# Kernel optimization log

Hardware: AMD Instinct MI355X
Metric: run time of the kernel (lower is better)

## Reference

```python
import jax, jax.numpy as jnp
import numpy as np

B, T, DIM = 4, 4096, 1024
HEADS, DIM_HEAD = 16, 64
INNER = HEADS * DIM_HEAD
SCALE = DIM_HEAD ** -0.5


def setup_inputs() -> dict:
    key = jax.random.key(0)
    k1, k2, k3, k4 = jax.random.split(key, 4)
    x = jax.random.normal(k1, (B, T, DIM), dtype=jnp.float32)
    mask = jax.random.bernoulli(k2, 0.2, (B, T))  # True = padding
    W_qkv = jax.random.normal(k3, (DIM, 3 * INNER), dtype=jnp.float32) * (DIM ** -0.5)
    W_out = jax.random.normal(k4, (INNER, DIM), dtype=jnp.float32) * (INNER ** -0.5)
    b_out = jnp.zeros((DIM,), dtype=jnp.float32)
    return {"x": x, "mask": mask, "W_qkv": W_qkv, "W_out": W_out, "b_out": b_out}


def reference(x, mask, W_qkv, W_out, b_out):
    Bs, Ts, _ = x.shape
    qkv = x @ W_qkv                                       # [B,T,3*inner]
    q, k, v = jnp.split(qkv, 3, axis=-1)
    # [B,T,H,Dh] -> [B,H,T,Dh]
    reshape = lambda t: t.reshape(Bs, Ts, HEADS, DIM_HEAD).transpose(0, 2, 1, 3)
    q, k, v = reshape(q), reshape(k), reshape(v)
    q = q * SCALE
    k = jax.nn.softmax(k, axis=-2)                        # softmax over sequence dim
    # zero out padded positions AFTER softmax (faithful to original)
    k = jnp.where(mask[:, None, :, None], 0.0, k)
    context = jnp.einsum('bhnd,bhne->bhde', k, v)         # [B,H,Dh,Dh]
    out = jnp.einsum('bhnd,bhde->bhne', q, context)       # [B,H,T,Dh]
    out = out.transpose(0, 2, 1, 3).reshape(Bs, Ts, INNER)
    return out @ W_out + b_out                            # dropout: eval mode (identity)
```

## Files before the change

kernel.cpp:

```cpp
#include <hip/hip_runtime.h>
#include <math.h>


typedef __bf16 bf16;
typedef __attribute__((ext_vector_type(4))) float f32x4;
typedef __attribute__((ext_vector_type(8))) __bf16 bf16x8;
typedef __attribute__((ext_vector_type(4))) __bf16 bf16x4;

#define SCALE_ 0.125f

__device__ __forceinline__ void g2l16(const void* g, void* l) {
  __builtin_amdgcn_global_load_lds((const __attribute__((address_space(1))) void*)g,
                                   (__attribute__((address_space(3))) void*)l, 16, 0, 0);
}

__global__ __launch_bounds__(256) void k_cvt(const float* __restrict__ in,
                                             bf16* __restrict__ out, int n4) {
  int i = blockIdx.x * 256 + threadIdx.x;
  if (i >= n4) return;
  f32x4 v = ((const f32x4*)in)[i];
  bf16x4 o;
  o[0] = (bf16)v[0]; o[1] = (bf16)v[1]; o[2] = (bf16)v[2]; o[3] = (bf16)v[3];
  ((bf16x4*)out)[i] = o;
}

__global__ __launch_bounds__(256) void k_trans(const float* __restrict__ W,
                                               bf16* __restrict__ Wt) {
  __shared__ float t[32][33];
  int n0 = blockIdx.x * 32, k0 = blockIdx.y * 32;
  int tx = threadIdx.x & 31, ty = threadIdx.x >> 5;
  #pragma unroll
  for (int s = 0; s < 4; s++) {
    int k = ty + s * 8;
    t[k][tx] = W[(size_t)(k0 + k) * 3072 + 1024 + n0 + tx];
  }
  __syncthreads();
  #pragma unroll
  for (int s = 0; s < 4; s++) {
    int n = ty + s * 8;
    Wt[(size_t)(n0 + n) * 1024 + k0 + tx] = (bf16)t[tx][n];
  }
}

__global__ __launch_bounds__(256) void k_wq(const float* __restrict__ W,
                                            bf16* __restrict__ wqs) {
  int idx = blockIdx.x * 256 + threadIdx.x;
  int i = idx >> 8, d4 = idx & 255;
  f32x4 v = *(const f32x4*)(W + (size_t)i * 3072 + d4 * 4);
  bf16x4 o;
  o[0] = (bf16)(v[0] * SCALE_); o[1] = (bf16)(v[1] * SCALE_);
  o[2] = (bf16)(v[2] * SCALE_); o[3] = (bf16)(v[3] * SCALE_);
  *(bf16x4*)(wqs + (size_t)i * 1024 + d4 * 4) = o;
}


__device__ __forceinline__ void stage_unit(const bf16* __restrict__ G, int base_row,
                                           int kcol, void* ldsBase, int tid) {
  #pragma unroll
  for (int r = 0; r < 2; ++r) {
    const int d  = tid * 16 + r * 8192;
    const int lb = d ^ (((d >> 7) & 3) << 4);
    g2l16(G + (size_t)(base_row + (lb >> 6)) * 1024 + kcol + ((lb & 63) >> 1),
          (char*)ldsBase + d);
  }
}

#define VM8() asm volatile("s_waitcnt vmcnt(8)" ::: "memory")

#define PHASE(DB, MH, KS, LOADB, ...)                                         \
  {                                                                           \
    const char* Ab_ = Lraw + (DB) * 65536 + (KS) * 16384;                     \
    _Pragma("unroll") for (int i_ = 0; i_ < 4; ++i_)                          \
      af[i_] = *(const bf16x8*)(Ab_ + aoff[MH][i_]);                          \
    if (LOADB) {                                                              \
      _Pragma("unroll") for (int j_ = 0; j_ < 4; ++j_)                        \
        bfr[j_] = *(const bf16x8*)(Ab_ + 32768 + boff[j_]);                   \
    }                                                                         \
    __VA_ARGS__;                                                              \
    __builtin_amdgcn_s_barrier();                                             \
    __builtin_amdgcn_s_setprio(1);                                            \
    _Pragma("unroll") for (int i_ = 0; i_ < 4; ++i_)                          \
      _Pragma("unroll") for (int j_ = 0; j_ < 4; ++j_)                        \
        acc[(MH) * 4 + i_][j_] = __builtin_amdgcn_mfma_f32_16x16x32_bf16(     \
            af[i_], bfr[j_], acc[(MH) * 4 + i_][j_], 0, 0, 0);                \
    __builtin_amdgcn_s_setprio(0);                                            \
    __builtin_amdgcn_s_barrier();                                             \
  }

__device__ __forceinline__ void gemm256_core(const bf16* __restrict__ A_,
                                             const bf16* __restrict__ B_,
                                             int row0, int col0,
                                             char* Lraw, f32x4 (&acc)[8][4]) {
  const int tid = threadIdx.x;
  const int wave = tid >> 6, lane = tid & 63, l16 = lane & 15, quad = lane >> 4;
  const int wr = wave >> 2, wc = wave & 3;
  int aoff[2][4], boff[4];
  #pragma unroll
  for (int mh = 0; mh < 2; ++mh)
    #pragma unroll
    for (int i = 0; i < 4; ++i) {
      const int row = wr * 128 + mh * 64 + i * 16 + l16;
      aoff[mh][i] = row * 64 + ((quad ^ ((row >> 1) & 3)) << 4);
    }
  #pragma unroll
  for (int j = 0; j < 4; ++j) {
    const int row = wc * 64 + j * 16 + l16;
    boff[j] = row * 64 + ((quad ^ ((row >> 1) & 3)) << 4);
  }
  bf16x8 af[4], bfr[4];
  stage_unit(A_, row0, 0,  Lraw + 0,      tid);
  stage_unit(B_, col0, 0,  Lraw + 32768,  tid);
  stage_unit(A_, row0, 32, Lraw + 16384,  tid);
  stage_unit(B_, col0, 32, Lraw + 49152,  tid);
  stage_unit(A_, row0, 64, Lraw + 65536,  tid);
  stage_unit(B_, col0, 64, Lraw + 98304,  tid);
  VM8();
  __builtin_amdgcn_s_barrier();
  for (int I = 0; I < 8; ++I) {
    const int k1 = (2 * I + 1) * 64, k2 = (2 * I + 2) * 64, k3 = (2 * I + 3) * 64;
    const bool pf = (I < 7);
    PHASE(0, 0, 0, true,  { stage_unit(A_, row0, k1 + 32, Lraw + 65536 + 16384, tid); })
    PHASE(0, 1, 0, false, { stage_unit(B_, col0, k1 + 32, Lraw + 65536 + 49152, tid); VM8(); })
    PHASE(0, 0, 1, true,  { if (pf) stage_unit(A_, row0, k2,      Lraw + 0,     tid); })
    PHASE(0, 1, 1, false, { if (pf) stage_unit(B_, col0, k2,      Lraw + 32768, tid); VM8(); })
    PHASE(1, 0, 0, true,  { if (pf) stage_unit(A_, row0, k2 + 32, Lraw + 16384, tid); })
    PHASE(1, 1, 0, false, { if (pf) stage_unit(B_, col0, k2 + 32, Lraw + 49152, tid); VM8(); })
    PHASE(1, 0, 1, true,  { if (pf) stage_unit(A_, row0, k3,      Lraw + 65536, tid); })
    PHASE(1, 1, 1, false, { if (pf) stage_unit(B_, col0, k3,      Lraw + 98304, tid); VM8(); })
  }
}

__global__ __launch_bounds__(512, 2) void k_gemm1(const bf16* __restrict__ A,
                                                  const bf16* __restrict__ Bt,
                                                  bf16* __restrict__ kv) {
  __shared__ __align__(16) char Lraw[131072];
  const int f = blockIdx.x, xcd = f & 7, w = f >> 3;
  const int row0 = (xcd * 8 + (w >> 3)) << 8;
  const int col0 = (w & 7) << 8;
  f32x4 acc[8][4] = {};
  gemm256_core(A, Bt, row0, col0, Lraw, acc);
  const int tid = threadIdx.x;
  const int wave = tid >> 6, lane = tid & 63, l16 = lane & 15, quad = lane >> 4;
  const int wr = wave >> 2, wc = wave & 3;
  #pragma unroll
  for (int ai = 0; ai < 8; ++ai) {
    const int gm0 = row0 + wr * 128 + ai * 16 + quad * 4;
    #pragma unroll
    for (int j = 0; j < 4; ++j) {
      const int gc = col0 + wc * 64 + j * 16 + l16;
      #pragma unroll
      for (int r = 0; r < 4; ++r)
        kv[(size_t)(gm0 + r) * 2048 + gc] = (bf16)acc[ai][j][r];
    }
  }
}

__global__ __launch_bounds__(256) void k_ctx(const bf16* __restrict__ kv,
                                             const int* __restrict__ mask,
                                             float* __restrict__ sumexp,
                                             float* __restrict__ ctx) {
  __shared__ float Lk[64][68];
  __shared__ float Lv[64][68];
  __shared__ float Sst[64][33];
  const int blk = blockIdx.x, tid = threadIdx.x;
  const int wave = tid >> 6, lane = tid & 63;
  const int ns = blk & 7, h = (blk >> 3) & 15, b = blk >> 7;
  const int d0 = (lane & 7) * 8, e0 = (lane >> 3) * 8;
  const int g = tid & 7;
  float acc[8][8] = {};
  float sum8[8] = {};
  const int nbase = ns * 512;
  for (int ch = 0; ch < 8; ++ch) {
    const int n0 = nbase + ch * 64;
    __syncthreads();
    #pragma unroll
    for (int it = 0; it < 2; ++it) {
      const int idx = it * 256 + tid;
      const int row = idx >> 3;
      const int gn = b * 4096 + n0 + row;
      const float m = mask[gn] ? 0.f : 1.f;
      bf16x8 t8 = *(const bf16x8*)(kv + (size_t)gn * 2048 + h * 64 + g * 8);
      float e[8];
      #pragma unroll
      for (int j = 0; j < 8; j++) { e[j] = __expf((float)t8[j]); sum8[j] += e[j]; }
      f32x4 lo, hi;
      lo[0] = e[0] * m; lo[1] = e[1] * m; lo[2] = e[2] * m; lo[3] = e[3] * m;
      hi[0] = e[4] * m; hi[1] = e[5] * m; hi[2] = e[6] * m; hi[3] = e[7] * m;
      *(f32x4*)&Lk[row][g * 8] = lo;
      *(f32x4*)&Lk[row][g * 8 + 4] = hi;
    }
    #pragma unroll
    for (int it = 0; it < 2; ++it) {
      const int idx = it * 256 + tid;
      const int row = idx >> 3;
      const int gn = b * 4096 + n0 + row;
      bf16x8 t8 = *(const bf16x8*)(kv + (size_t)gn * 2048 + 1024 + h * 64 + g * 8);
      f32x4 lo, hi;
      lo[0] = (float)t8[0]; lo[1] = (float)t8[1]; lo[2] = (float)t8[2]; lo[3] = (float)t8[3];
      hi[0] = (float)t8[4]; hi[1] = (float)t8[5]; hi[2] = (float)t8[6]; hi[3] = (float)t8[7];
      *(f32x4*)&Lv[row][g * 8] = lo;
      *(f32x4*)&Lv[row][g * 8 + 4] = hi;
    }
    __syncthreads();
    #pragma unroll 4
    for (int t = 0; t < 16; t++) {
      const int n = (wave << 4) + t;
      f32x4 ka = *(const f32x4*)&Lk[n][d0];
      f32x4 kb = *(const f32x4*)&Lk[n][d0 + 4];
      f32x4 va = *(const f32x4*)&Lv[n][e0];
      f32x4 vb = *(const f32x4*)&Lv[n][e0 + 4];
      float kk[8] = {ka[0], ka[1], ka[2], ka[3], kb[0], kb[1], kb[2], kb[3]};
      float vv[8] = {va[0], va[1], va[2], va[3], vb[0], vb[1], vb[2], vb[3]};
      #pragma unroll
      for (int a = 0; a < 8; a++)
        #pragma unroll
        for (int c = 0; c < 8; c++) acc[a][c] += kk[a] * vv[c];
    }
  }
  __syncthreads();
  float* r0 = &Lk[0][0];
  float* r1 = &Lv[0][0];
  if (wave < 2) {
    float* r = wave ? r1 : r0;
    #pragma unroll
    for (int a = 0; a < 8; a++)
      #pragma unroll
      for (int c = 0; c < 8; c++) r[(d0 + a) * 64 + e0 + c] = acc[a][c];
  }
  {
    const int rg = tid >> 3;
    #pragma unroll
    for (int j = 0; j < 8; j++) Sst[g * 8 + j][rg] = sum8[j];
  }
  __syncthreads();
  if (wave >= 2) {
    float* r = (wave == 3) ? r1 : r0;
    #pragma unroll
    for (int a = 0; a < 8; a++)
      #pragma unroll
      for (int c = 0; c < 8; c++) r[(d0 + a) * 64 + e0 + c] += acc[a][c];
  } else if (tid < 64) {
    float s = 0.f;
    #pragma unroll 8
    for (int rg = 0; rg < 32; rg++) s += Sst[tid][rg];
    atomicAdd(&sumexp[b * 1024 + h * 64 + tid], s);
  }
  __syncthreads();
  float* cbase = ctx + ((size_t)(b * 16 + h) << 12);
  for (int i = tid; i < 4096; i += 256) atomicAdd(cbase + i, r0[i] + r1[i]);
}

__global__ __launch_bounds__(256) void k_m2(const float* __restrict__ ctx,
                                            const float* __restrict__ sumexp,
                                            const float* __restrict__ Wout,
                                            bf16* __restrict__ M2t) {
  __shared__ float Lc[64][64];
  __shared__ float Linv[64];
  const int b = blockIdx.z, h = blockIdx.y, jt = blockIdx.x;
  const int tid = threadIdx.x, dg = tid >> 6, jl = tid & 63;
  const float* cbase = ctx + ((size_t)(b * 16 + h) << 12);
  for (int i = tid; i < 4096; i += 256) (&Lc[0][0])[i] = cbase[i];
  if (tid < 64) Linv[tid] = 1.f / sumexp[b * 1024 + h * 64 + tid];
  __syncthreads();
  float acc[4][16] = {};
  const int j0 = jt * 256 + jl;
  for (int e = 0; e < 64; e++) {
    const float* wrow = Wout + (size_t)(h * 64 + e) * 1024 + j0;
    float w0 = wrow[0], w1 = wrow[64], w2 = wrow[128], w3 = wrow[192];
    #pragma unroll
    for (int dd = 0; dd < 16; dd++) {
      float c = Lc[dg * 16 + dd][e];
      acc[0][dd] += c * w0; acc[1][dd] += c * w1;
      acc[2][dd] += c * w2; acc[3][dd] += c * w3;
    }
  }
  #pragma unroll
  for (int jj = 0; jj < 4; jj++) {
    const size_t jrow = ((size_t)b << 20) + (size_t)(jt * 256 + jl + jj * 64) * 1024 + h * 64 + dg * 16;
    #pragma unroll
    for (int dd = 0; dd < 16; dd++)
      M2t[jrow + dd] = (bf16)(acc[jj][dd] * Linv[dg * 16 + dd]);
  }
}

__global__ __launch_bounds__(256) void k_m3(const bf16* __restrict__ M2t,
                                            const bf16* __restrict__ wqs,
                                            bf16* __restrict__ M3t) {
  __shared__ __align__(16) bf16 As[128 * 32];
  __shared__ __align__(16) bf16 Bs[128 * 32];
  const int tid = threadIdx.x;
  const int wave = tid >> 6, lane = tid & 63, l16 = lane & 15, quad = lane >> 4;
  const int wm = (wave >> 1) << 6, wn = (wave & 1) << 6;
  const int row0 = blockIdx.y << 7, col0 = blockIdx.x << 7;
  const bf16* A  = M2t + ((size_t)blockIdx.z << 20);
  bf16*       C  = M3t + ((size_t)blockIdx.z << 20);
  f32x4 acc[4][4] = {};
  for (int kt = 0; kt < 1024; kt += 32) {
    #pragma unroll
    for (int it = 0; it < 2; ++it) {
      const int cb = (wave * 2 + it) * 64;
      const int c = cb + lane;
      const int m = c >> 2, k8 = (c & 3) * 8;
      g2l16(A   + (size_t)(row0 + m) * 1024 + kt + k8, As + cb * 8);
      g2l16(wqs + (size_t)(col0 + m) * 1024 + kt + k8, Bs + cb * 8);
    }
    __syncthreads();
    bf16x8 af[4], bfr[4];
    #pragma unroll
    for (int i = 0; i < 4; i++) af[i]  = *(const bf16x8*)(As + (wm + i * 16 + l16) * 32 + quad * 8);
    #pragma unroll
    for (int j = 0; j < 4; j++) bfr[j] = *(const bf16x8*)(Bs + (wn + j * 16 + l16) * 32 + quad * 8);
    #pragma unroll
    for (int i = 0; i < 4; i++)
      #pragma unroll
      for (int j = 0; j < 4; j++)
        acc[i][j] = __builtin_amdgcn_mfma_f32_16x16x32_bf16(af[i], bfr[j], acc[i][j], 0, 0, 0);
    __syncthreads();
  }
  #pragma unroll
  for (int i = 0; i < 4; i++) {
    const int gm0 = row0 + wm + i * 16 + quad * 4;
    #pragma unroll
    for (int j = 0; j < 4; j++) {
      const int gc = col0 + wn + j * 16 + l16;
      #pragma unroll
      for (int r = 0; r < 4; r++)
        C[(size_t)(gm0 + r) * 1024 + gc] = (bf16)acc[i][j][r];
    }
  }
}

__global__ __launch_bounds__(512, 2) void k_gemm2(const bf16* __restrict__ A,
                                                  const bf16* __restrict__ M3t,
                                                  const float* __restrict__ bias,
                                                  float* __restrict__ out) {
  __shared__ __align__(16) char Lraw[131072];
  const int f = blockIdx.x, xcd = f & 7, w = f >> 3;
  const int row0 = (xcd * 8 + (w >> 2)) << 8;
  const int col0 = (w & 3) << 8;
  const bf16* Bt = M3t + ((size_t)(row0 >> 12) << 20);
  f32x4 acc[8][4] = {};
  gemm256_core(A, Bt, row0, col0, Lraw, acc);
  const int tid = threadIdx.x;
  const int wave = tid >> 6, lane = tid & 63, l16 = lane & 15, quad = lane >> 4;
  const int wr = wave >> 2, wc = wave & 3;
  float bj[4];
  #pragma unroll
  for (int j = 0; j < 4; j++) bj[j] = bias[col0 + wc * 64 + j * 16 + l16];
  #pragma unroll
  for (int ai = 0; ai < 8; ++ai) {
    const int gm0 = row0 + wr * 128 + ai * 16 + quad * 4;
    #pragma unroll
    for (int j = 0; j < 4; ++j) {
      const int gc = col0 + wc * 64 + j * 16 + l16;
      #pragma unroll
      for (int r = 0; r < 4; ++r)
        out[(size_t)(gm0 + r) * 1024 + gc] = acc[ai][j][r] + bj[j];
    }
  }
}

extern "C" void kernel_launch(void* const* d_in, const int* in_sizes, int n_in,
                              void* d_out, int out_size, void* d_ws, size_t ws_size,
                              hipStream_t stream) {
  const float* x    = (const float*)d_in[0];
  const int*   mask = (const int*)d_in[1];
  const float* Wqkv = (const float*)d_in[2];
  const float* Wout = (const float*)d_in[3];
  const float* bout = (const float*)d_in[4];
  float* out = (float*)d_out;
  char* ws = (char*)d_ws;
  bf16*  xb     = (bf16*)(ws);
  bf16*  wt     = (bf16*)(ws + 33554432);
  bf16*  wqs    = (bf16*)(ws + 37748736);
  bf16*  kv     = (bf16*)(ws + 39845888);
  float* sumexp = (float*)(ws + 106954752);
  float* ctx    = (float*)(ws + 106971136);
  bf16*  m2t    = (bf16*)(ws + 108019712);
  bf16*  m3t    = (bf16*)(ws + 116408320);

  hipMemsetAsync(sumexp, 0, 16384 + 1048576, stream);
  k_cvt  <<<16384, 256, 0, stream>>>(x, xb, 4194304);
  k_trans<<<dim3(64, 32), 256, 0, stream>>>(Wqkv, wt);
  k_wq   <<<1024, 256, 0, stream>>>(Wqkv, wqs);
  k_gemm1<<<512, 512, 0, stream>>>(xb, wt, kv);
  k_ctx  <<<512, 256, 0, stream>>>(kv, mask, sumexp, ctx);
  k_m2   <<<dim3(4, 16, 4), 256, 0, stream>>>(ctx, sumexp, Wout, m2t);
  k_m3   <<<dim3(8, 8, 4), 256, 0, stream>>>(m2t, wqs, m3t);
  k_gemm2<<<256, 512, 0, stream>>>(xb, m3t, bout, out);
}
```

Measured before the change: 326.0 us.

## Double-buffer LDS fragment registers to overlap ds_reads with MFMA in GEMM core

Restructures the 256x256 GEMM main loop so LDS fragment loads for the next phase are issued into a second register bank while MFMAs run on the current bank. Explicit lgkmcnt waits with sched barriers and finer vmcnt waits replace the earlier load-then-barrier-then-compute phases. The goal is to hide LDS read latency behind matrix-core work. In exchange it uses more VGPRs, which could cause spills or lower occupancy under the 512x2 launch bounds, and the hand-tuned wait counts must stay correct.

```diff
diff --git a/kernel.cpp b/kernel.cpp
--- a/kernel.cpp
+++ b/kernel.cpp
@@ -65,27 +65,81 @@
   }
 }
 
-#define VM8() asm volatile("s_waitcnt vmcnt(8)" ::: "memory")
-
-#define PHASE(DB, MH, KS, LOADB, ...)                                         \
-  {                                                                           \
-    const char* Ab_ = Lraw + (DB) * 65536 + (KS) * 16384;                     \
+#define VM(n) asm volatile("s_waitcnt vmcnt(" #n ")" ::: "memory")
+#define LG(n) do { asm volatile("s_waitcnt lgkmcnt(" #n ")" ::: "memory"); \
+                   __builtin_amdgcn_sched_barrier(0); } while (0)
+
+#define DSA(bank, DB, MH, KS)                                                 \
+  { const char* p_ = Lraw + (DB) * 65536 + (KS) * 16384;                      \
     _Pragma("unroll") for (int i_ = 0; i_ < 4; ++i_)                          \
-      af[i_] = *(const bf16x8*)(Ab_ + aoff[MH][i_]);                          \
-    if (LOADB) {                                                              \
-      _Pragma("unroll") for (int j_ = 0; j_ < 4; ++j_)                        \
-        bfr[j_] = *(const bf16x8*)(Ab_ + 32768 + boff[j_]);                   \
-    }                                                                         \
-    __VA_ARGS__;                                                              \
-    __builtin_amdgcn_s_barrier();                                             \
-    __builtin_amdgcn_s_setprio(1);                                            \
-    _Pragma("unroll") for (int i_ = 0; i_ < 4; ++i_)                          \
-      _Pragma("unroll") for (int j_ = 0; j_ < 4; ++j_)                        \
-        acc[(MH) * 4 + i_][j_] = __builtin_amdgcn_mfma_f32_16x16x32_bf16(     \
-            af[i_], bfr[j_], acc[(MH) * 4 + i_][j_], 0, 0, 0);                \
-    __builtin_amdgcn_s_setprio(0);                                            \
-    __builtin_amdgcn_s_barrier();                                             \
-  }
+      bank[i_] = *(const bf16x8*)(p_ + aoff[MH][i_]); }
+#define DSB(bank, DB, KS)                                                     \
+  { const char* p_ = Lraw + (DB) * 65536 + 32768 + (KS) * 16384;              \
+    _Pragma("unroll") for (int j_ = 0; j_ < 4; ++j_)                          \
+      bank[j_] = *(const bf16x8*)(p_ + boff[j_]); }
+
+#define MFMA16(AF, BF, MH)                                                    \
+  __builtin_amdgcn_s_setprio(1);                                              \
+  _Pragma("unroll") for (int i_ = 0; i_ < 4; ++i_)                            \
+    _Pragma("unroll") for (int j_ = 0; j_ < 4; ++j_)                          \
+      acc[(MH) * 4 + i_][j_] = __builtin_amdgcn_mfma_f32_16x16x32_bf16(       \
+          AF[i_], BF[j_], acc[(MH) * 4 + i_][j_], 0, 0, 0);                   \
+  __builtin_amdgcn_s_setprio(0)
+
+#define BAR() __builtin_amdgcn_s_barrier()
+
+#define GITER(PF, KB)                                                         \
+                        \
+  VM(4);                                                                      \
+  stage_unit(A_, row0, (KB) + 96, Lraw + 65536 + 16384, tid);                 \
+  DSA(af_b, 0, 1, 0);                                                         \
+  LG(4);                                                                      \
+  MFMA16(af_a, bf_a, 0);                                                      \
+  BAR();                                                                      \
+                                              \
+  stage_unit(B_, col0, (KB) + 96, Lraw + 65536 + 49152, tid);                 \
+  DSA(af_a, 0, 0, 1); DSB(bf_b, 0, 1);                                        \
+  LG(8);                                                                      \
+  MFMA16(af_b, bf_a, 1);                                                      \
+  BAR();                                                                      \
+                                                   \
+  VM(4);                                                                      \
+  if (PF) stage_unit(A_, row0, (KB) + 128, Lraw + 0, tid);                    \
+  DSA(af_b, 0, 1, 1);                                                         \
+  LG(4);                                                                      \
+  MFMA16(af_a, bf_b, 0);                                                      \
+  BAR();                                                                      \
+                                       \
+  if (PF) stage_unit(B_, col0, (KB) + 128, Lraw + 32768, tid);                \
+  DSA(af_a, 1, 0, 0); DSB(bf_a, 1, 0);                                        \
+  LG(8);                                                                      \
+  MFMA16(af_b, bf_b, 1);                                                      \
+  BAR();                                                                      \
+                                                   \
+  if (PF) { VM(4); } else { VM(0); }                                          \
+  if (PF) stage_unit(A_, row0, (KB) + 160, Lraw + 16384, tid);                \
+  DSA(af_b, 1, 1, 0);                                                         \
+  LG(4);                                                                      \
+  MFMA16(af_a, bf_a, 0);                                                      \
+  BAR();                                                                      \
+                                              \
+  if (PF) stage_unit(B_, col0, (KB) + 160, Lraw + 49152, tid);                \
+  DSA(af_a, 1, 0, 1); DSB(bf_b, 1, 1);                                        \
+  LG(8);                                                                      \
+  MFMA16(af_b, bf_a, 1);                                                      \
+  BAR();                                                                      \
+                                                   \
+  if (PF) { VM(4); }                                                          \
+  if (PF) stage_unit(A_, row0, (KB) + 192, Lraw + 65536, tid);                \
+  DSA(af_b, 1, 1, 1);                                                         \
+  LG(4);                                                                      \
+  MFMA16(af_a, bf_b, 0);                                                      \
+  BAR();                                                                      \
+                                  \
+  if (PF) stage_unit(B_, col0, (KB) + 192, Lraw + 98304, tid);                \
+  if (PF) { DSA(af_a, 0, 0, 0); DSB(bf_a, 0, 0); LG(8); } else { LG(0); }     \
+  MFMA16(af_b, bf_b, 1);                                                      \
+  if (PF) BAR();
 
 __device__ __forceinline__ void gemm256_core(const bf16* __restrict__ A_,
                                              const bf16* __restrict__ B_,
@@ -107,27 +161,22 @@
     const int row = wc * 64 + j * 16 + l16;
     boff[j] = row * 64 + ((quad ^ ((row >> 1) & 3)) << 4);
   }
-  bf16x8 af[4], bfr[4];
+  bf16x8 af_a[4], af_b[4], bf_a[4], bf_b[4];
   stage_unit(A_, row0, 0,  Lraw + 0,      tid);
   stage_unit(B_, col0, 0,  Lraw + 32768,  tid);
   stage_unit(A_, row0, 32, Lraw + 16384,  tid);
   stage_unit(B_, col0, 32, Lraw + 49152,  tid);
   stage_unit(A_, row0, 64, Lraw + 65536,  tid);
   stage_unit(B_, col0, 64, Lraw + 98304,  tid);
-  VM8();
-  __builtin_amdgcn_s_barrier();
-  for (int I = 0; I < 8; ++I) {
-    const int k1 = (2 * I + 1) * 64, k2 = (2 * I + 2) * 64, k3 = (2 * I + 3) * 64;
-    const bool pf = (I < 7);
-    PHASE(0, 0, 0, true,  { stage_unit(A_, row0, k1 + 32, Lraw + 65536 + 16384, tid); })
-    PHASE(0, 1, 0, false, { stage_unit(B_, col0, k1 + 32, Lraw + 65536 + 49152, tid); VM8(); })
-    PHASE(0, 0, 1, true,  { if (pf) stage_unit(A_, row0, k2,      Lraw + 0,     tid); })
-    PHASE(0, 1, 1, false, { if (pf) stage_unit(B_, col0, k2,      Lraw + 32768, tid); VM8(); })
-    PHASE(1, 0, 0, true,  { if (pf) stage_unit(A_, row0, k2 + 32, Lraw + 16384, tid); })
-    PHASE(1, 1, 0, false, { if (pf) stage_unit(B_, col0, k2 + 32, Lraw + 49152, tid); VM8(); })
-    PHASE(1, 0, 1, true,  { if (pf) stage_unit(A_, row0, k3,      Lraw + 65536, tid); })
-    PHASE(1, 1, 1, false, { if (pf) stage_unit(B_, col0, k3,      Lraw + 98304, tid); VM8(); })
-  }
+  VM(8);
+  BAR();
+  DSA(af_a, 0, 0, 0);
+  DSB(bf_a, 0, 0);
+  for (int t = 0; t < 7; ++t) {
+    const int KB = t * 128;
+    GITER(1, KB)
+  }
+  GITER(0, 896)
 }
 
 __global__ __launch_bounds__(512, 2) void k_gemm1(const bf16* __restrict__ A,
```

Measured after the change: 331.4 us. Within noise of the previous version (+1.7%).
